# Performance work log

Hardware: AMD Instinct MI355X
Metric: run time of the kernel (lower is better)

## Reference

```python
import jax, jax.numpy as jnp
import numpy as np

S, FEAT, D, H, L, DFF, C = 1024, 64, 512, 8, 2, 2048, 10
DB = D // 4  # distance-bias MLP hidden
NFREQ = D // 6  # 85 -> 6*85=510 dims, padded to 512
EPS = 1e-5


def _layernorm(x, g, b):
    mu = jnp.mean(x, axis=-1, keepdims=True)
    var = jnp.mean(jnp.square(x - mu), axis=-1, keepdims=True)
    return (x - mu) * jax.lax.rsqrt(var + EPS) * g + b


def setup_inputs() -> dict:
    key = jax.random.key(0)
    ks = iter(jax.random.split(key, 40))
    def w(shape, scale=0.02):
        return (jax.random.normal(next(ks), shape, jnp.float32) * scale)
    inp = {
        'features': jax.random.normal(next(ks), (S, FEAT), jnp.float32),
        'positions': jax.random.uniform(next(ks), (S, 3), jnp.float32),
        'freq_bands': jnp.asarray(10.0 ** np.linspace(0.0, 10.0, NFREQ), jnp.float32),
        'in_w': w((FEAT, D)), 'in_b': jnp.zeros((D,), jnp.float32),
        'qw': w((L, D, D)), 'qb': jnp.zeros((L, D), jnp.float32),
        'kw': w((L, D, D)), 'kb': jnp.zeros((L, D), jnp.float32),
        'vw': w((L, D, D)), 'vb': jnp.zeros((L, D), jnp.float32),
        'ow': w((L, D, D)), 'ob': jnp.zeros((L, D), jnp.float32),
        'db1w': w((L, 1, DB), 0.5), 'db1b': jnp.zeros((L, DB), jnp.float32),
        'db2w': w((L, DB, H), 0.1), 'db2b': jnp.zeros((L, H), jnp.float32),
        'n1g': jnp.ones((L, D), jnp.float32), 'n1b': jnp.zeros((L, D), jnp.float32),
        'n2g': jnp.ones((L, D), jnp.float32), 'n2b': jnp.zeros((L, D), jnp.float32),
        'f1w': w((L, D, DFF)), 'f1b': jnp.zeros((L, DFF), jnp.float32),
        'f2w': w((L, DFF, D)), 'f2b': jnp.zeros((L, D), jnp.float32),
        'c1w': w((D, D // 2)), 'c1b': jnp.zeros((D // 2,), jnp.float32),
        'c2w': w((D // 2, C)), 'c2b': jnp.zeros((C,), jnp.float32),
    }
    return inp


def _forward(features, positions, freq_bands, in_w, in_b, qw, qb, kw, kb, vw, vb,
             ow, ob, db1w, db1b, db2w, db2b, n1g, n1b, n2g, n2b,
             f1w, f1b, f2w, f2b, c1w, c1b, c2w, c2b):
    d_model = in_w.shape[1]
    nhead = db2w.shape[-1]
    head_dim = d_model // nhead
    scale = 1.0 / np.sqrt(head_dim)

    x = features[None] @ in_w + in_b            # [1, S, D]
    pos = positions[None]                        # [1, S, 3]

    # 3D sinusoidal positional encoding: [sin0,cos0,sin1,cos1,sin2,cos2]
    enc = []
    for i in range(3):
        cs = pos[..., i:i + 1] * freq_bands      # [1, S, NFREQ] (broadcast)
        enc.append(jnp.sin(cs))
        enc.append(jnp.cos(cs))
    pe = jnp.concatenate(enc, axis=-1)           # [1, S, 6*NFREQ]
    if pe.shape[-1] > d_model:
        pe = pe[..., :d_model]
    elif pe.shape[-1] < d_model:
        pe = jnp.pad(pe, ((0, 0), (0, 0), (0, d_model - pe.shape[-1])))
    x = x + pe

    # pairwise distances [1, S, S, 1]; safe sqrt (zero grad on diagonal)
    diff = pos[:, :, None, :] - pos[:, None, :, :]
    sq = jnp.sum(jnp.square(diff), axis=-1, keepdims=True)
    dist = jnp.sqrt(jnp.where(sq > 0, sq, 1.0)) * (sq > 0)

    n_layers = qw.shape[0]
    seq = x.shape[1]
    for l in range(n_layers):
        q = (x @ qw[l] + qb[l]).reshape(1, seq, nhead, head_dim)
        k = (x @ kw[l] + kb[l]).reshape(1, seq, nhead, head_dim)
        v = (x @ vw[l] + vb[l]).reshape(1, seq, nhead, head_dim)
        scores = jnp.einsum('bihd,bjhd->bhij', q, k) * scale  # [1,H,S,S]
        hbias = jax.nn.relu(dist @ db1w[l] + db1b[l])          # [1,S,S,DB]
        bias = jnp.einsum('bijc,ch->bhij', hbias, db2w[l]) + db2b[l][None, :, None, None]
        attn = jax.nn.softmax(scores + bias, axis=-1)
        out = jnp.einsum('bhij,bjhd->bihd', attn, v).reshape(1, seq, d_model)
        out = out @ ow[l] + ob[l]
        x = _layernorm(x + out, n1g[l], n1b[l])
        ffn = jax.nn.relu(x @ f1w[l] + f1b[l]) @ f2w[l] + f2b[l]
        x = _layernorm(x + ffn, n2g[l], n2b[l])

    pooled = jnp.mean(x, axis=1)                 # [1, D]
    return jax.nn.relu(pooled @ c1w + c1b) @ c2w + c2b  # [1, C]


def reference(features, positions, freq_bands, in_w, in_b, qw, qb, kw, kb, vw, vb,
              ow, ob, db1w, db1b, db2w, db2b, n1g, n1b, n2g, n2b,
              f1w, f1b, f2w, f2b, c1w, c1b, c2w, c2b):
    return _forward(features, positions, freq_bands, in_w, in_b, qw, qb, kw, kb, vw, vb,
                    ow, ob, db1w, db1b, db2w, db2b, n1g, n1b, n2g, n2b,
                    f1w, f1b, f2w, f2b, c1w, c1b, c2w, c2b)
```

## Files before the change

kernel.cpp:

```cpp
#include <hip/hip_runtime.h>

namespace {
constexpr int kS   = 1024;
constexpr int kD   = 512;
constexpr int kDFF = 2048;
constexpr int kNF  = 85;
}

typedef __attribute__((ext_vector_type(8))) short bhalf8_t;
typedef _Float16 half8_t __attribute__((ext_vector_type(8)));
typedef __attribute__((ext_vector_type(4))) float f32x4_t;

__device__ __forceinline__ float wave_sum(float v) {
#pragma unroll
    for (int o = 1; o < 64; o <<= 1) v += __shfl_xor(v, o, 64);
    return v;
}
__device__ __forceinline__ unsigned short f2h(float f) {
    _Float16 h = (_Float16)f;
    return __builtin_bit_cast(unsigned short, h);
}
__device__ __forceinline__ float h2f(unsigned short u) {
    return (float)__builtin_bit_cast(_Float16, u);
}

__global__ __launch_bounds__(256)
void prep_a_k(const float* __restrict__ feat, const float* __restrict__ pos,
              const float* __restrict__ fb, const float* __restrict__ in_w,
              const float* __restrict__ in_b, float* __restrict__ x,
              unsigned short* __restrict__ xb,
              float* __restrict__ dist,
              const float* __restrict__ a_, const float* __restrict__ b_,
              float* __restrict__ bp_out)
{
    __shared__ float smem[128];
    int bid = blockIdx.x;
    int t = threadIdx.x;
    if (bid < 1024) {
        int s = bid;
        if (t < 64) smem[t] = feat[s * 64 + t];
        __syncthreads();
        float acc0 = in_b[t], acc1 = in_b[t + 256];
#pragma unroll 8
        for (int c = 0; c < 64; ++c) {
            float fv = smem[c];
            acc0 = fmaf(fv, in_w[c * kD + t], acc0);
            acc1 = fmaf(fv, in_w[c * kD + 256 + t], acc1);
        }
        float pe0 = 0.f, pe1 = 0.f;
        {
            int d = t;
            if (d < 6 * kNF) {
                int seg = d / kNF, idx = d - seg * kNF;
                float cs = pos[s * 3 + (seg >> 1)] * fb[idx];
                pe0 = (seg & 1) ? cosf(cs) : sinf(cs);
            }
            d = t + 256;
            if (d < 6 * kNF) {
                int seg = d / kNF, idx = d - seg * kNF;
                float cs = pos[s * 3 + (seg >> 1)] * fb[idx];
                pe1 = (seg & 1) ? cosf(cs) : sinf(cs);
            }
        }
        float o0 = acc0 + pe0, o1 = acc1 + pe1;
        x[s * kD + t]        = o0;
        x[s * kD + 256 + t]  = o1;
        xb[s * kD + t]       = f2h(o0);
        xb[s * kD + 256 + t] = f2h(o1);
    } else if (bid < 2048) {
        int i = bid - 1024;
        float px = pos[i * 3], py = pos[i * 3 + 1], pz = pos[i * 3 + 2];
        for (int j = t; j < kS; j += 256) {
            float dx = px - pos[j * 3], dy = py - pos[j * 3 + 1], dz = pz - pos[j * 3 + 2];
            float sq = dx * dx + dy * dy + dz * dz;
            dist[(long)i * kS + j] = sq > 0.f ? sqrtf(sq) : 0.f;
        }
    } else {
        int l = bid - 2048;
        const float* ap = a_ + l * 128;
        const float* bp = b_ + l * 128;
        float* out = bp_out + l * 128;
        if (t < 128) {
            float a = ap[t], b = bp[t];
            smem[t] = (a != 0.f) ? (-b / a) : 3.0e38f;
        }
        __syncthreads();
        for (int ksz = 2; ksz <= 128; ksz <<= 1) {
            for (int j = ksz >> 1; j > 0; j >>= 1) {
                if (t < 128) {
                    int ixj = t ^ j;
                    if (ixj > t) {
                        bool up = ((t & ksz) == 0);
                        float x0 = smem[t], x1 = smem[ixj];
                        if ((x0 > x1) == up) { smem[t] = x1; smem[ixj] = x0; }
                    }
                }
                __syncthreads();
            }
        }
        if (t < 128) out[t] = smem[t];
    }
}

__device__ __forceinline__ void tr_tile32(const float* __restrict__ in,
                                          unsigned short* __restrict__ out,
                                          int N, int K, int k0, int n0, int t,
                                          float* tile )
{
    int r = t >> 3, c4 = (t & 7) * 4;
    float4 v = *reinterpret_cast<const float4*>(&in[(long)(k0 + r) * N + n0 + c4]);
    tile[r * 33 + c4] = v.x; tile[r * 33 + c4 + 1] = v.y;
    tile[r * 33 + c4 + 2] = v.z; tile[r * 33 + c4 + 3] = v.w;
    __syncthreads();
    int nr = t >> 3, kq = (t & 7) * 4;
    unsigned short h[4];
#pragma unroll
    for (int j = 0; j < 4; ++j) h[j] = f2h(tile[(kq + j) * 33 + nr]);
    *reinterpret_cast<ushort4*>(&out[(long)(n0 + nr) * K + k0 + kq]) =
        make_ushort4(h[0], h[1], h[2], h[3]);
}

__global__ __launch_bounds__(256)
void prep_w_k(const float* __restrict__ qw, const float* __restrict__ kw,
              const float* __restrict__ vw, const float* __restrict__ ow,
              unsigned short* __restrict__ qwb, unsigned short* __restrict__ kwb,
              unsigned short* __restrict__ vwb, unsigned short* __restrict__ owb,
              const float* __restrict__ f1w, unsigned short* __restrict__ f1wb,
              const float* __restrict__ f2w, unsigned short* __restrict__ f2wb,
              const float* __restrict__ a_, const float* __restrict__ b_,
              const float* __restrict__ w2, const float* __restrict__ b2,
              const float* __restrict__ bp, float* __restrict__ Atab,
              float* __restrict__ Btab)
{
    __shared__ float smem[32 * 33];
    int bid = blockIdx.x;
    int t = threadIdx.x;
    if (bid < 2048) {
        int zz = bid >> 8, rem = bid & 255;
        int mat = zz >> 1, layer = zz & 1;
        const float* in = (mat == 0) ? qw : (mat == 1) ? kw : (mat == 2) ? vw : ow;
        unsigned short* out = (mat == 0) ? qwb : (mat == 1) ? kwb : (mat == 2) ? vwb : owb;
        tr_tile32(in + (long)layer * 262144, out + (long)layer * 262144,
                  512, 512, (rem & 15) * 32, (rem >> 4) * 32, t, smem);
    } else if (bid < 4096) {
        int l = bid - 2048;
        int z = l >> 10;
        tr_tile32(f1w + (long)z * 1048576, f1wb + (long)z * 1048576,
                  2048, 512, (l & 15) * 32, ((l >> 4) & 63) * 32, t, smem);
    } else if (bid < 6144) {
        int l = bid - 4096;
        int z = l >> 10;
        tr_tile32(f2w + (long)z * 1048576, f2wb + (long)z * 1048576,
                  512, 2048, (l & 63) * 32, ((l >> 6) & 15) * 32, t, smem);
    } else {
        int l = bid - 6144;
        int seg = l % 129, ly = l / 129;
        const float* ap = a_ + ly * 128;
        const float* bpp = b_ + ly * 128;
        const float* w2p = w2 + ly * 1024;
        const float* b2p = b2 + ly * 8;
        const float* bpl = bp + ly * 128;
        float* At = Atab + ly * 1040;
        float* Bt = Btab + ly * 1040;

        float m;
        if (seg == 0)        m = bpl[0] - 1.0f;
        else if (seg == 128) m = bpl[127] + 1.0f;
        else                 m = 0.5f * (bpl[seg - 1] + bpl[seg]);

        int h = t & 7, cg = t >> 3;
        float A = 0.f, B = 0.f;
#pragma unroll
        for (int j = 0; j < 4; ++j) {
            int c = cg * 4 + j;
            float a = ap[c], b = bpp[c];
            if (fmaf(a, m, b) > 0.f) {
                float w = w2p[c * 8 + h];
                A = fmaf(a, w, A);
                B = fmaf(b, w, B);
            }
        }
#pragma unroll
        for (int off = 8; off < 64; off <<= 1) {
            A += __shfl_xor(A, off, 64);
            B += __shfl_xor(B, off, 64);
        }
        int w = t >> 6, lane = t & 63;
        if (lane < 8) { smem[w * 8 + lane] = A; smem[32 + w * 8 + lane] = B; }
        __syncthreads();
        if (t < 8) {
            float At_ = smem[t] + smem[8 + t] + smem[16 + t] + smem[24 + t];
            float Bt_ = smem[32 + t] + smem[40 + t] + smem[48 + t] + smem[56 + t];
            At[seg * 8 + t] = At_;
            Bt[seg * 8 + t] = Bt_ + b2p[t];
        }
    }
}

constexpr int BKp = 72;
constexpr int ASZ = 64 * BKp;
constexpr int BSZ = 128 * BKp;

template<int K>
__device__ __forceinline__ void gemm_core(
    const unsigned short* __restrict__ Ap, const unsigned short* __restrict__ Bp,
    int lda, int ldb, int bm, int bn, int tid,
    unsigned short* __restrict__ As, unsigned short* __restrict__ Bs,
    f32x4_t acc[2][4])
{
    int w = tid >> 6, lane = tid & 63, quad = lane >> 4, l16 = lane & 15;
    int wm = (w >> 1) * 32, wn = (w & 1) * 64;
    int ar = tid >> 2, ac = (tid & 3) * 16;
    int br = tid >> 1, bc = (tid & 1) * 32;
    const unsigned short* pa = Ap + (long)(bm + ar) * lda + ac;
    const unsigned short* pb = Bp + (long)(bn + br) * ldb + bc;

    bhalf8_t a0_0, a0_1, b0_0, b0_1, b0_2, b0_3;
    bhalf8_t a1_0, a1_1, b1_0, b1_1, b1_2, b1_3;

#define LDG(S, k0) do { \
    a##S##_0 = *reinterpret_cast<const bhalf8_t*>(pa + (k0)); \
    a##S##_1 = *reinterpret_cast<const bhalf8_t*>(pa + (k0) + 8); \
    b##S##_0 = *reinterpret_cast<const bhalf8_t*>(pb + (k0)); \
    b##S##_1 = *reinterpret_cast<const bhalf8_t*>(pb + (k0) + 8); \
    b##S##_2 = *reinterpret_cast<const bhalf8_t*>(pb + (k0) + 16); \
    b##S##_3 = *reinterpret_cast<const bhalf8_t*>(pb + (k0) + 24); } while (0)
#define STG(S, as, bs) do { \
    *reinterpret_cast<bhalf8_t*>(&(as)[ar * BKp + ac])      = a##S##_0; \
    *reinterpret_cast<bhalf8_t*>(&(as)[ar * BKp + ac + 8])  = a##S##_1; \
    *reinterpret_cast<bhalf8_t*>(&(bs)[br * BKp + bc])      = b##S##_0; \
    *reinterpret_cast<bhalf8_t*>(&(bs)[br * BKp + bc + 8])  = b##S##_1; \
    *reinterpret_cast<bhalf8_t*>(&(bs)[br * BKp + bc + 16]) = b##S##_2; \
    *reinterpret_cast<bhalf8_t*>(&(bs)[br * BKp + bc + 24]) = b##S##_3; } while (0)

    constexpr int NT = K / 64;
    LDG(0, 0);
    STG(0, As, Bs);
    if (NT > 1) LDG(1, 64);
#pragma unroll
    for (int t = 0; t < NT; ++t) {
        __syncthreads();
        if (t + 2 < NT) {
            if ((t & 1) == 0) LDG(0, (t + 2) * 64);
            else              LDG(1, (t + 2) * 64);
        }
        const unsigned short* as = As + (t & 1) * ASZ;
        const unsigned short* bs = Bs + (t & 1) * BSZ;
#pragma unroll
        for (int kq = 0; kq < 2; ++kq) {
            bhalf8_t af[2], bf[4];
#pragma unroll
            for (int i = 0; i < 2; ++i)
                af[i] = *reinterpret_cast<const bhalf8_t*>(
                    &as[(wm + i * 16 + l16) * BKp + kq * 32 + quad * 8]);
#pragma unroll
            for (int j = 0; j < 4; ++j)
                bf[j] = *reinterpret_cast<const bhalf8_t*>(
                    &bs[(wn + j * 16 + l16) * BKp + kq * 32 + quad * 8]);
#pragma unroll
            for (int i = 0; i < 2; ++i)
#pragma unroll
                for (int j = 0; j < 4; ++j)
                    acc[i][j] = __builtin_amdgcn_mfma_f32_16x16x32_f16(
                        __builtin_bit_cast(half8_t, af[i]), __builtin_bit_cast(half8_t, bf[j]),
                        acc[i][j], 0, 0, 0);
        }
        if (t + 1 < NT) {
            if (((t + 1) & 1) == 0) STG(0, As, Bs);
            else                    STG(1, As + ASZ, Bs + BSZ);
        }
    }
#undef LDG
#undef STG
}

__global__ __launch_bounds__(256, 2)
void qkv_bias_k(const unsigned short* __restrict__ xb,
                const unsigned short* __restrict__ qwb, const unsigned short* __restrict__ kwb,
                const unsigned short* __restrict__ vwb,
                const float* __restrict__ qbias, const float* __restrict__ kbias,
                const float* __restrict__ vbias,
                unsigned short* __restrict__ qb2, unsigned short* __restrict__ kb2,
                unsigned short* __restrict__ vtb,
                const float* __restrict__ dist, const float* __restrict__ bp,
                const float* __restrict__ Atab, const float* __restrict__ Btab,
                unsigned short* __restrict__ bmap, unsigned int* __restrict__ cnt)
{
    __shared__ __align__(16) unsigned short smem[2 * ASZ + 2 * BSZ];
    int bid = blockIdx.x;
    int tid = threadIdx.x;
    if (bid < 192) {
        int z = bid >> 6, rem = bid & 63;
        int bm = (rem & 15) * 64, bn = (rem >> 4) * 128;
        const unsigned short* Bp = (z == 1) ? kwb : (z == 2) ? vwb : qwb;
        const float* bias = (z == 1) ? kbias : (z == 2) ? vbias : qbias;
        f32x4_t acc[2][4] = {};
        gemm_core<512>(xb, Bp, 512, 512, bm, bn, tid, smem, smem + 2 * ASZ, acc);

        int w = tid >> 6, lane = tid & 63, quad = lane >> 4, l16 = lane & 15;
        int wm = (w >> 1) * 32, wn = (w & 1) * 64;
        if (z == 2) {
            __syncthreads();
            unsigned short* T = smem;
#pragma unroll
            for (int j = 0; j < 4; ++j) {
                int ln = wn + j * 16 + l16;
                float bv = bias[bn + ln];
#pragma unroll
                for (int i = 0; i < 2; ++i)
#pragma unroll
                    for (int r = 0; r < 4; ++r)
                        T[ln * BKp + wm + i * 16 + quad * 4 + r] =
                            f2h((acc[i][j][r] + bv) * 1024.f);
            }
            __syncthreads();
            int nr = tid >> 1, mc = (tid & 1) * 32;
            int gn = bn + nr;
            unsigned short* dst = vtb + (long)(gn >> 6) * 65536
                                + (long)(gn & 63) * 1024 + bm + mc;
#pragma unroll
            for (int jj = 0; jj < 4; ++jj)
                *reinterpret_cast<bhalf8_t*>(dst + jj * 8) =
                    *reinterpret_cast<const bhalf8_t*>(&T[nr * BKp + mc + jj * 8]);
        } else {
#pragma unroll
            for (int j = 0; j < 4; ++j) {
                int n = bn + wn + j * 16 + l16;
                float bv = bias[n];
                unsigned short* dst = ((z == 1) ? kb2 : qb2)
                    + (long)(n >> 6) * 131072 + (n & 63);
#pragma unroll
                for (int i = 0; i < 2; ++i)
#pragma unroll
                    for (int r = 0; r < 4; ++r) {
                        int m = bm + wm + i * 16 + quad * 4 + r;
                        float s = acc[i][j][r] + bv;
                        unsigned short hi = f2h(s);
                        dst[(long)m * 128]      = hi;
                        dst[(long)m * 128 + 64] = (z == 0) ? f2h(s - h2f(hi)) : hi;
                    }
            }
        }
    } else {
        if (bid == 192 && tid < 8) cnt[tid] = 0;
        float* fs = reinterpret_cast<float*>(smem);
        float* bps = fs;
        float* Ah  = fs + 128;
        float* Bh  = fs + 1160;
        int t = tid;
        if (t < 128) bps[t] = bp[t];
        for (int i = t; i < 1032; i += 256) { Ah[i] = Atab[i]; Bh[i] = Btab[i]; }
        __syncthreads();
        long i = ((long)(bid - 192) * 256 + t) * 4;
        float4 d4 = *reinterpret_cast<const float4*>(dist + i);
        float dv[4] = {d4.x, d4.y, d4.z, d4.w};
        int seg[4];
#pragma unroll
        for (int j = 0; j < 4; ++j) {
            float tv = dv[j];
            int lo = 0, hi = 128;
            while (lo < hi) { int mid = (lo + hi) >> 1; if (bps[mid] < tv) lo = mid + 1; else hi = mid; }
            seg[j] = lo;
        }
#pragma unroll
        for (int h = 0; h < 8; ++h) {
            unsigned short o[4];
#pragma unroll
            for (int j = 0; j < 4; ++j)
                o[j] = f2h(fmaf(Ah[seg[j] * 8 + h], dv[j], Bh[seg[j] * 8 + h]));
            *reinterpret_cast<ushort4*>(bmap + (long)h * 1048576 + i) =
                make_ushort4(o[0], o[1], o[2], o[3]);
        }
    }
}

__global__ __launch_bounds__(256, 2)
void bgemm_ffn1_k(const unsigned short* __restrict__ A,
                  const unsigned short* __restrict__ B,
                  const float* __restrict__ bias,
                  unsigned short* __restrict__ hb)
{
    __shared__ __align__(16) unsigned short smem[2 * ASZ + 2 * BSZ];
    int tid = threadIdx.x;
    int bm = blockIdx.x * 64, bn = blockIdx.y * 128;
    f32x4_t acc[2][4] = {};
    gemm_core<512>(A, B, 512, 512, bm, bn, tid, smem, smem + 2 * ASZ, acc);

    int w = tid >> 6, lane = tid & 63, quad = lane >> 4, l16 = lane & 15;
    int wm = (w >> 1) * 32, wn = (w & 1) * 64;
#pragma unroll
    for (int j = 0; j < 4; ++j) {
        int n = bn + wn + j * 16 + l16;
        float bv = bias[n];
#pragma unroll
        for (int i = 0; i < 2; ++i)
#pragma unroll
            for (int r = 0; r < 4; ++r) {
                int m = bm + wm + i * 16 + quad * 4 + r;
                hb[(long)m * kDFF + n] = f2h(fmaxf(acc[i][j][r] + bv, 0.f));
            }
    }
}

template<int K>
__global__ __launch_bounds__(256, 2)
void bgemm_k(const unsigned short* __restrict__ A, const unsigned short* __restrict__ B,
             int N, int lda, int ldb, unsigned short* __restrict__ Cpart)
{
    __shared__ __align__(16) unsigned short smem[2 * ASZ + 2 * BSZ];
    int tid = threadIdx.x;
    int ks = blockIdx.z;
    const unsigned short* Ap = A + (long)ks * K;
    const unsigned short* Bp = B + (long)ks * K;
    int bm = blockIdx.x * 64, bn = blockIdx.y * 128;
    f32x4_t acc[2][4] = {};
    gemm_core<K>(Ap, Bp, lda, ldb, bm, bn, tid, smem, smem + 2 * ASZ, acc);

    int w = tid >> 6, lane = tid & 63, quad = lane >> 4, l16 = lane & 15;
    int wm = (w >> 1) * 32, wn = (w & 1) * 64;
    unsigned short* Cp = Cpart + (long)ks * kS * N;
#pragma unroll
    for (int i = 0; i < 2; ++i)
#pragma unroll
        for (int j = 0; j < 4; ++j)
#pragma unroll
            for (int r = 0; r < 4; ++r) {
                int m = bm + wm + i * 16 + quad * 4 + r;
                int n = bn + wn + j * 16 + l16;
                Cp[(long)m * N + n] = f2h(acc[i][j][r]);
            }
}

__global__ __launch_bounds__(64)
void flash_part_k(const unsigned short* __restrict__ qb2, const unsigned short* __restrict__ kb2,
                  const unsigned short* __restrict__ vtb, const unsigned short* __restrict__ bmap,
                  unsigned short* __restrict__ po, float* __restrict__ pm, float* __restrict__ pl)
{
    __shared__ unsigned short Ps[16 * 136];

    int tid = threadIdx.x;
    int wg  = blockIdx.x;
    int lin = (wg & 7) * 512 + (wg >> 3);
    int qb  = lin & 63;
    int h   = (lin >> 6) & 7;
    int z   = lin >> 9;
    int bm = qb * 16;
    int k0 = z * 128;

    const unsigned short* Qh = qb2 + (long)h * 131072;
    const unsigned short* Kh = kb2 + (long)h * 131072;
    const unsigned short* Vh = vtb + (long)h * 65536;
    const unsigned short* Bm = bmap + (long)h * 1048576;

    int quad = tid >> 4, l16 = tid & 15;

    bhalf8_t aq[4];
#pragma unroll
    for (int kq = 0; kq < 4; ++kq)
        aq[kq] = *reinterpret_cast<const bhalf8_t*>(
            &Qh[(long)(bm + l16) * 128 + kq * 32 + quad * 8]);

    f32x4_t sacc[8] = {};
#pragma unroll
    for (int kq = 0; kq < 4; ++kq) {
        bhalf8_t bk[8];
#pragma unroll
        for (int nb = 0; nb < 8; ++nb)
            bk[nb] = *reinterpret_cast<const bhalf8_t*>(
                &Kh[(long)(k0 + nb * 16 + l16) * 128 + kq * 32 + quad * 8]);
#pragma unroll
        for (int nb = 0; nb < 8; ++nb)
            sacc[nb] = __builtin_amdgcn_mfma_f32_16x16x32_f16(
                __builtin_bit_cast(half8_t, aq[kq]), __builtin_bit_cast(half8_t, bk[nb]),
                sacc[nb], 0, 0, 0);
    }

    float m_r[4] = {-3.0e38f, -3.0e38f, -3.0e38f, -3.0e38f};
#pragma unroll
    for (int nb = 0; nb < 8; ++nb)
#pragma unroll
        for (int r = 0; r < 4; ++r) {
            int gm = bm + quad * 4 + r;
            int gn = k0 + nb * 16 + l16;
            float bias = h2f(Bm[(long)gm * kS + gn]);
            float s = fmaf(sacc[nb][r], 0.125f, bias);
            sacc[nb][r] = s;
            m_r[r] = fmaxf(m_r[r], s);
        }
#pragma unroll
    for (int r = 0; r < 4; ++r) {
        float m_ = m_r[r];
#pragma unroll
        for (int off = 1; off < 16; off <<= 1) m_ = fmaxf(m_, __shfl_xor(m_, off, 64));
        m_r[r] = m_;
    }

    float l_r[4];
#pragma unroll
    for (int r = 0; r < 4; ++r) {
        int row = quad * 4 + r;
        float mN = m_r[r];
        float s_ = 0.f;
#pragma unroll
        for (int nb = 0; nb < 8; ++nb) {
            float p = __expf(sacc[nb][r] - mN);
            Ps[row * 136 + nb * 16 + l16] = f2h(p * 16384.f);
            s_ += p;
        }
#pragma unroll
        for (int off = 1; off < 16; off <<= 1) s_ += __shfl_xor(s_, off, 64);
        l_r[r] = s_;
    }

    long sbase = (((long)z * 8 + h) * 64 + qb) * 16;
    if (l16 == 0) {
#pragma unroll
        for (int r = 0; r < 4; ++r) {
            pm[sbase + quad * 4 + r] = m_r[r];
            pl[sbase + quad * 4 + r] = l_r[r];
        }
    }
    __syncthreads();

    f32x4_t oacc[4] = {};
#pragma unroll
    for (int kq2 = 0; kq2 < 4; ++kq2) {
        bhalf8_t ap = *reinterpret_cast<const bhalf8_t*>(&Ps[l16 * 136 + kq2 * 32 + quad * 8]);
#pragma unroll
        for (int j2 = 0; j2 < 4; ++j2) {
            bhalf8_t bv = *reinterpret_cast<const bhalf8_t*>(
                &Vh[(long)(j2 * 16 + l16) * 1024 + k0 + kq2 * 32 + quad * 8]);
            oacc[j2] = __builtin_amdgcn_mfma_f32_16x16x32_f16(
                __builtin_bit_cast(half8_t, ap), __builtin_bit_cast(half8_t, bv),
                oacc[j2], 0, 0, 0);
        }
    }

    unsigned short* pob = po + sbase * 64;
#pragma unroll
    for (int j2 = 0; j2 < 4; ++j2)
#pragma unroll
        for (int r = 0; r < 4; ++r)
            pob[(quad * 4 + r) * 64 + j2 * 16 + l16] =
                f2h(oacc[j2][r] * (1.f / 16777216.f));
}

__global__ __launch_bounds__(256)
void flash_merge_k(const unsigned short* __restrict__ po, const float* __restrict__ pm,
                   const float* __restrict__ pl, unsigned short* __restrict__ aob)
{
    int t = blockIdx.x * 256 + threadIdx.x;
    int c8  = t & 7;
    int row = (t >> 3) & 15;
    int qb  = (t >> 7) & 63;
    int h   = t >> 13;
    long sidx = (((long)h * 64) + qb) * 16 + row;

    float m[8];
    float M = -3.0e38f;
#pragma unroll
    for (int z = 0; z < 8; ++z) { m[z] = pm[z * 8192 + sidx]; M = fmaxf(M, m[z]); }
    float w[8], lt = 0.f;
#pragma unroll
    for (int z = 0; z < 8; ++z) {
        w[z] = __expf(m[z] - M);
        lt = fmaf(pl[z * 8192 + sidx], w[z], lt);
    }
    float acc[8] = {};
#pragma unroll
    for (int z = 0; z < 8; ++z) {
        const unsigned short* p = po + (z * 8192 + sidx) * 64 + c8 * 8;
        ushort4 a = *reinterpret_cast<const ushort4*>(p);
        ushort4 b = *reinterpret_cast<const ushort4*>(p + 4);
        acc[0] = fmaf(h2f(a.x), w[z], acc[0]); acc[1] = fmaf(h2f(a.y), w[z], acc[1]);
        acc[2] = fmaf(h2f(a.z), w[z], acc[2]); acc[3] = fmaf(h2f(a.w), w[z], acc[3]);
        acc[4] = fmaf(h2f(b.x), w[z], acc[4]); acc[5] = fmaf(h2f(b.y), w[z], acc[5]);
        acc[6] = fmaf(h2f(b.z), w[z], acc[6]); acc[7] = fmaf(h2f(b.w), w[z], acc[7]);
    }
    float inv = 1.f / lt;
    unsigned short hi[8];
#pragma unroll
    for (int j = 0; j < 8; ++j) hi[j] = f2h(acc[j] * inv);
    long base = ((long)qb * 16 + row) * 512 + h * 64 + c8 * 8;
    *reinterpret_cast<ushort4*>(&aob[base])     = make_ushort4(hi[0], hi[1], hi[2], hi[3]);
    *reinterpret_cast<ushort4*>(&aob[base + 4]) = make_ushort4(hi[4], hi[5], hi[6], hi[7]);
}

__global__ __launch_bounds__(256)
void add_ln_fused_k(const unsigned short* __restrict__ part, float* __restrict__ x,
                    const float* __restrict__ bias,
                    const float* __restrict__ g, const float* __restrict__ b,
                    unsigned short* __restrict__ xb, int splitk)
{
    __shared__ float sm[4];
    int row = blockIdx.x, t = threadIdx.x;
    const long MN = (long)kS * kD;
    float* xr = x + (long)row * kD;
    float s0 = 0.f, s1 = 0.f;
    const unsigned short* pr = part + (long)row * kD;
    for (int sl = 0; sl < splitk; ++sl) {
        s0 += h2f(pr[(long)sl * MN + t]);
        s1 += h2f(pr[(long)sl * MN + t + 256]);
    }
    s0 += bias[t] + xr[t];
    s1 += bias[t + 256] + xr[t + 256];
    float sum = wave_sum(s0 + s1);
    if ((t & 63) == 0) sm[t >> 6] = sum;
    __syncthreads();
    sum = sm[0] + sm[1] + sm[2] + sm[3];
    float mu = sum * (1.f / kD);
    float d0 = s0 - mu, d1 = s1 - mu;
    __syncthreads();
    float vs = wave_sum(d0 * d0 + d1 * d1);
    if ((t & 63) == 0) sm[t >> 6] = vs;
    __syncthreads();
    vs = sm[0] + sm[1] + sm[2] + sm[3];
    float rs = rsqrtf(vs * (1.f / kD) + 1e-5f);
    float o0 = fmaf(d0 * rs, g[t], b[t]);
    float o1 = fmaf(d1 * rs, g[t + 256], b[t + 256]);
    xr[t]       = o0;
    xr[t + 256] = o1;
    unsigned short* xrow = xb + (long)row * 512;
    xrow[t]       = f2h(o0);
    xrow[t + 256] = f2h(o1);
}

__global__ __launch_bounds__(256)
void pool_head_k(const float* __restrict__ x, float* __restrict__ partial,
                 unsigned int* __restrict__ cnt2,
                 const float* __restrict__ c1w, const float* __restrict__ c1b,
                 const float* __restrict__ c2w, const float* __restrict__ c2b,
                 float* __restrict__ out)
{
    __shared__ float pooled[kD];
    __shared__ float h1[256];
    __shared__ int isLast;
    int t = threadIdx.x;
    int cb = blockIdx.x & 1, rb = blockIdx.x >> 1;
    int col = cb * 256 + t;
    float s = 0.f;
    for (int r = rb * 128; r < rb * 128 + 128; ++r) s += x[(long)r * kD + col];
    partial[rb * kD + col] = s;

    __threadfence();
    if (t == 0) isLast = (atomicAdd(cnt2, 1u) == 15u);
    __syncthreads();
    if (!isLast) return;
    __threadfence();

    for (int d = t; d < kD; d += 256) {
        float ps = 0.f;
        for (int r = 0; r < 8; ++r) ps += partial[r * kD + d];
        pooled[d] = ps * (1.0f / kS);
    }
    __syncthreads();
    float acc = c1b[t];
    for (int f = 0; f < kD; ++f) acc = fmaf(pooled[f], c1w[f * 256 + t], acc);
    h1[t] = fmaxf(acc, 0.f);
    __syncthreads();
    if (t < 10) {
        float o = c2b[t];
        for (int f = 0; f < 256; ++f) o = fmaf(h1[f], c2w[f * 10 + t], o);
        out[t] = o;
    }
}

extern "C" void kernel_launch(void* const* d_in, const int* in_sizes, int n_in,
                              void* d_out, int out_size, void* d_ws, size_t ws_size,
                              hipStream_t stream)
{
    (void)in_sizes; (void)n_in; (void)out_size; (void)ws_size;
    const float* features = (const float*)d_in[0];
    const float* positions= (const float*)d_in[1];
    const float* fb       = (const float*)d_in[2];
    const float* in_w     = (const float*)d_in[3];
    const float* in_b     = (const float*)d_in[4];
    const float* qw  = (const float*)d_in[5];
    const float* qb  = (const float*)d_in[6];
    const float* kw  = (const float*)d_in[7];
    const float* kb  = (const float*)d_in[8];
    const float* vw  = (const float*)d_in[9];
    const float* vb  = (const float*)d_in[10];
    const float* ow  = (const float*)d_in[11];
    const float* ob  = (const float*)d_in[12];
    const float* db1w= (const float*)d_in[13];
    const float* db1b= (const float*)d_in[14];
    const float* db2w= (const float*)d_in[15];
    const float* db2b= (const float*)d_in[16];
    const float* n1g = (const float*)d_in[17];
    const float* n1b = (const float*)d_in[18];
    const float* n2g = (const float*)d_in[19];
    const float* n2b = (const float*)d_in[20];
    const float* f1w = (const float*)d_in[21];
    const float* f1b = (const float*)d_in[22];
    const float* f2w = (const float*)d_in[23];
    const float* f2b = (const float*)d_in[24];
    const float* c1w = (const float*)d_in[25];
    const float* c1b = (const float*)d_in[26];
    const float* c2w = (const float*)d_in[27];
    const float* c2b = (const float*)d_in[28];

    float* ws = (float*)d_ws;
    const long SD = (long)kS * kD;
    float* x      = ws;
    float* dist   = ws + 3 * SD;
    float* part_f = ws + 5 * SD;
    float* bpw    = ws + 17 * SD;
    float* Atab   = bpw + 256;
    float* Btab   = Atab + 2080;
    float* partial= Btab + 2080;

    unsigned short* part16 = (unsigned short*)part_f;
    unsigned short* po     = (unsigned short*)part_f;
    float* pmv = part_f + 4194304 / 2 + 65536;
    float* plv = pmv + 65536;
    unsigned int* cnt2 = (unsigned int*)(plv + 65536);

    unsigned short* ub = (unsigned short*)(ws + 17 * SD + 8512);
    unsigned short* xb   = ub;
    unsigned short* aob  = xb   + 524288;
    unsigned short* qb2  = aob  + 524288;
    unsigned short* kb2  = qb2  + 1048576;
    unsigned short* vtb  = kb2  + 1048576;
    unsigned short* hb   = vtb  + 524288;
    unsigned short* qwb  = hb   + 2097152;
    unsigned short* kwb  = qwb  + 524288;
    unsigned short* vwb  = kwb  + 524288;
    unsigned short* owb  = vwb  + 524288;
    unsigned short* f1wb = owb  + 524288;
    unsigned short* f2wb = f1wb + 2097152;
    unsigned short* bmap = f2wb + 2097152;

    prep_a_k<<<2050, 256, 0, stream>>>(features, positions, fb, in_w, in_b, x, xb,
                                       dist, db1w, db1b, bpw);
    prep_w_k<<<6402, 256, 0, stream>>>(qw, kw, vw, ow, qwb, kwb, vwb, owb,
                                       f1w, f1wb, f2w, f2wb,
                                       db1w, db1b, db2w, db2b, bpw, Atab, Btab);

    for (int l = 0; l < 2; ++l) {
        qkv_bias_k<<<1216, 256, 0, stream>>>(
            xb, qwb + l * 262144, kwb + l * 262144, vwb + l * 262144,
            qb + l * kD, kb + l * kD, vb + l * kD, qb2, kb2, vtb,
            dist, bpw + l * 128, Atab + l * 1040, Btab + l * 1040, bmap, cnt2);

        flash_part_k<<<4096, 64, 0, stream>>>(
            qb2, kb2, vtb, bmap, po, pmv, plv);
        flash_merge_k<<<256, 256, 0, stream>>>(po, pmv, plv, aob);

        bgemm_k<128><<<dim3(16, 4, 4), 256, 0, stream>>>(
            aob, owb + l * 262144, 512, 512, 512, part16);
        add_ln_fused_k<<<kS, 256, 0, stream>>>(
            part16, x, ob + l * kD, n1g + l * kD, n1b + l * kD, xb, 4);

        bgemm_ffn1_k<<<dim3(16, 16), 256, 0, stream>>>(
            xb, f1wb + l * 1048576, f1b + l * kDFF, hb);

        bgemm_k<512><<<dim3(16, 4, 4), 256, 0, stream>>>(
            hb, f2wb + l * 1048576, 512, 2048, 2048, part16);
        add_ln_fused_k<<<kS, 256, 0, stream>>>(
            part16, x, f2b + l * kD, n2g + l * kD, n2b + l * kD, xb, 4);
    }

    pool_head_k<<<16, 256, 0, stream>>>(x, partial, cnt2, c1w, c1b, c2w, c2b,
                                        (float*)d_out);
}
```

Baseline: 310.0 us.

## Share K/V tiles across four query-block waves in LDS and permute bias map layout

```diff
diff --git a/kernel.cpp b/kernel.cpp
--- a/kernel.cpp
+++ b/kernel.cpp
@@ -362,14 +362,17 @@
             while (lo < hi) { int mid = (lo + hi) >> 1; if (bps[mid] < tv) lo = mid + 1; else hi = mid; }
             seg[j] = lo;
         }
+        long gm  = i >> 10;
+        int gn0  = (int)(i & 1023);
+        int zz   = gn0 >> 7, nb = (gn0 >> 4) & 7, c4 = gn0 & 15;
+        long pbase = gm * 1024 + zz * 128 + nb;
 #pragma unroll
         for (int h = 0; h < 8; ++h) {
-            unsigned short o[4];
+            unsigned short* bh = bmap + (long)h * 1048576 + pbase;
 #pragma unroll
             for (int j = 0; j < 4; ++j)
-                o[j] = f2h(fmaf(Ah[seg[j] * 8 + h], dv[j], Bh[seg[j] * 8 + h]));
-            *reinterpret_cast<ushort4*>(bmap + (long)h * 1048576 + i) =
-                make_ushort4(o[0], o[1], o[2], o[3]);
+                bh[(c4 + j) * 8] =
+                    f2h(fmaf(Ah[seg[j] * 8 + h], dv[j], Bh[seg[j] * 8 + h]));
         }
     }
 }
@@ -431,34 +434,61 @@
             }
 }
 
-__global__ __launch_bounds__(64)
+__global__ __launch_bounds__(256, 3)
 void flash_part_k(const unsigned short* __restrict__ qb2, const unsigned short* __restrict__ kb2,
                   const unsigned short* __restrict__ vtb, const unsigned short* __restrict__ bmap,
                   unsigned short* __restrict__ po, float* __restrict__ pm, float* __restrict__ pl)
 {
-    __shared__ unsigned short Ps[16 * 136];
+    constexpr int KP = 136;
+    __shared__ __align__(16) unsigned short Klds[128 * KP];
+    __shared__ __align__(16) unsigned short Vlds[64 * KP];
 
     int tid = threadIdx.x;
+    int w    = tid >> 6;
+    int lane = tid & 63;
+    int quad = lane >> 4, l16 = lane & 15;
+
     int wg  = blockIdx.x;
-    int lin = (wg & 7) * 512 + (wg >> 3);
-    int qb  = lin & 63;
-    int h   = (lin >> 6) & 7;
-    int z   = lin >> 9;
-    int bm = qb * 16;
-    int k0 = z * 128;
+    int lin = (wg & 7) * 128 + (wg >> 3);
+    int qbg = lin & 15;
+    int h   = (lin >> 4) & 7;
+    int z   = lin >> 7;
+    int qb  = qbg * 4 + w;
+    int bm  = qb * 16;
+    int k0  = z * 128;
 
     const unsigned short* Qh = qb2 + (long)h * 131072;
     const unsigned short* Kh = kb2 + (long)h * 131072;
     const unsigned short* Vh = vtb + (long)h * 65536;
     const unsigned short* Bm = bmap + (long)h * 1048576;
 
-    int quad = tid >> 4, l16 = tid & 15;
+    {
+        int kr = tid >> 1, kc = (tid & 1) * 64;
+#pragma unroll
+        for (int j = 0; j < 8; ++j)
+            *reinterpret_cast<bhalf8_t*>(&Klds[kr * KP + kc + j * 8]) =
+                *reinterpret_cast<const bhalf8_t*>(&Kh[(long)(k0 + kr) * 128 + kc + j * 8]);
+        int vr = tid >> 2, vc = (tid & 3) * 32;
+#pragma unroll
+        for (int j = 0; j < 4; ++j)
+            *reinterpret_cast<bhalf8_t*>(&Vlds[vr * KP + vc + j * 8]) =
+                *reinterpret_cast<const bhalf8_t*>(&Vh[(long)vr * 1024 + k0 + vc + j * 8]);
+    }
 
     bhalf8_t aq[4];
 #pragma unroll
     for (int kq = 0; kq < 4; ++kq)
         aq[kq] = *reinterpret_cast<const bhalf8_t*>(
             &Qh[(long)(bm + l16) * 128 + kq * 32 + quad * 8]);
+    bhalf8_t bias8[4];
+#pragma unroll
+    for (int r = 0; r < 4; ++r) {
+        int gm = bm + quad * 4 + r;
+        bias8[r] = *reinterpret_cast<const bhalf8_t*>(
+            &Bm[(long)gm * 1024 + z * 128 + l16 * 8]);
+    }
+
+    __syncthreads();
 
     f32x4_t sacc[8] = {};
 #pragma unroll
@@ -467,7 +497,7 @@
 #pragma unroll
         for (int nb = 0; nb < 8; ++nb)
             bk[nb] = *reinterpret_cast<const bhalf8_t*>(
-                &Kh[(long)(k0 + nb * 16 + l16) * 128 + kq * 32 + quad * 8]);
+                &Klds[(nb * 16 + l16) * KP + kq * 32 + quad * 8]);
 #pragma unroll
         for (int nb = 0; nb < 8; ++nb)
             sacc[nb] = __builtin_amdgcn_mfma_f32_16x16x32_f16(
@@ -480,9 +510,7 @@
     for (int nb = 0; nb < 8; ++nb)
 #pragma unroll
         for (int r = 0; r < 4; ++r) {
-            int gm = bm + quad * 4 + r;
-            int gn = k0 + nb * 16 + l16;
-            float bias = h2f(Bm[(long)gm * kS + gn]);
+            float bias = h2f((unsigned short)bias8[r][nb]);
             float s = fmaf(sacc[nb][r], 0.125f, bias);
             sacc[nb][r] = s;
             m_r[r] = fmaxf(m_r[r], s);
@@ -495,6 +523,9 @@
         m_r[r] = m_;
     }
 
+    __syncthreads();
+
+    unsigned short* Ps = Klds + w * 16 * KP;
     float l_r[4];
 #pragma unroll
     for (int r = 0; r < 4; ++r) {
@@ -504,7 +535,7 @@
 #pragma unroll
         for (int nb = 0; nb < 8; ++nb) {
             float p = __expf(sacc[nb][r] - mN);
-            Ps[row * 136 + nb * 16 + l16] = f2h(p * 16384.f);
+            Ps[row * KP + nb * 16 + l16] = f2h(p * 16384.f);
             s_ += p;
         }
 #pragma unroll
@@ -520,16 +551,15 @@
             pl[sbase + quad * 4 + r] = l_r[r];
         }
     }
-    __syncthreads();
 
     f32x4_t oacc[4] = {};
 #pragma unroll
     for (int kq2 = 0; kq2 < 4; ++kq2) {
-        bhalf8_t ap = *reinterpret_cast<const bhalf8_t*>(&Ps[l16 * 136 + kq2 * 32 + quad * 8]);
+        bhalf8_t ap = *reinterpret_cast<const bhalf8_t*>(&Ps[l16 * KP + kq2 * 32 + quad * 8]);
 #pragma unroll
         for (int j2 = 0; j2 < 4; ++j2) {
             bhalf8_t bv = *reinterpret_cast<const bhalf8_t*>(
-                &Vh[(long)(j2 * 16 + l16) * 1024 + k0 + kq2 * 32 + quad * 8]);
+                &Vlds[(j2 * 16 + l16) * KP + kq2 * 32 + quad * 8]);
             oacc[j2] = __builtin_amdgcn_mfma_f32_16x16x32_f16(
                 __builtin_bit_cast(half8_t, ap), __builtin_bit_cast(half8_t, bv),
                 oacc[j2], 0, 0, 0);
@@ -743,7 +773,7 @@
             qb + l * kD, kb + l * kD, vb + l * kD, qb2, kb2, vtb,
             dist, bpw + l * 128, Atab + l * 1040, Btab + l * 1040, bmap, cnt2);
 
-        flash_part_k<<<4096, 64, 0, stream>>>(
+        flash_part_k<<<1024, 256, 0, stream>>>(
             qb2, kb2, vtb, bmap, po, pmv, plv);
         flash_merge_k<<<256, 256, 0, stream>>>(po, pmv, plv, aob);
 
```

Result: faster. 289.6 us (-6.6%).
